# Optimization experiments

Measured on AMD Instinct MI355X. Metric: run time of the kernel, lower is better.

The kernel has to match this reference:

```python
import jax, jax.numpy as jnp
import numpy as np

DIST_THRESH = 0.1
W_DIST = 0.05
W_CHAMFER = 0.05
W_SEP = 0.0005


def setup_inputs() -> dict:
    key = jax.random.key(0)
    k1, k2, k3, k4 = jax.random.split(key, 4)
    B, N, K = 4, 200000, 64
    return {
        "landmarks_C": jax.random.uniform(k1, (B, N, 3), jnp.float32),          # predicted point coords
        "landmarks_F": jax.random.normal(k2, (B, N, 4), jnp.float32) * 0.05,    # [dist, dx, dy, dz]
        "targets_C": jax.random.uniform(k3, (B, K, 3), jnp.float32),            # GT landmark coords
        "targets_F": jax.random.randint(k4, (B, K), 0, 8),                      # GT landmark class labels
        "classes": jnp.arange(6),                                               # classes to supervise
    }


def reference(landmarks_C, landmarks_F, targets_C, targets_F, classes):
    def per_batch(C_i, F_i, tC, tF):
        # class mask over GT landmarks (replaces boolean indexing in torch)
        mask_k = jnp.any(tF[None, :] == classes[:, None], axis=0)          # [K]
        n_valid = mask_k.sum()
        dists_i = F_i[:, 0]                                                # predicted distance, [N]
        coords_i = C_i + F_i[:, 1:]                                        # refined coords, [N,3]
        # pairwise dists GT landmarks -> raw point coords, invalid classes pushed to +inf
        pd = jnp.linalg.norm(C_i[None, :, :] - tC[:, None, :], axis=-1)    # [K,N]
        pd = jnp.where(mask_k[:, None], pd, jnp.inf)
        min_d = pd.min(axis=0)                                             # [N]
        pm = min_d < DIST_THRESH                                           # points near some GT landmark
        # smooth-L1 (beta=1, sum) on predicted distance; clip(inf)=2*thresh reproduces empty-target fallback
        tgt = jnp.clip(min_d, 0.0, 2.0 * DIST_THRESH)
        diff = dists_i - tgt
        ad = jnp.abs(diff)
        dist_loss = jnp.where(ad < 1.0, 0.5 * diff * diff, ad - 0.5).sum()
        # pairwise dists GT landmarks -> refined coords
        ld = jnp.linalg.norm(coords_i[None, :, :] - tC[:, None, :], axis=-1)  # [K,N]
        ld_m = jnp.where(mask_k[:, None], ld, jnp.inf)
        p2g = jnp.where(pm, ld_m.min(axis=0), 0.0)                         # pred->gt, masked points only
        g2p = jnp.where(mask_k, ld_m.min(axis=1), 0.0)                     # gt->pred, valid GT only
        chamfer = (p2g * p2g).sum() + (g2p * g2p).sum()
        # separation: ratio of dists to 2 nearest (valid) GT landmarks, per masked point
        _, idx = jax.lax.top_k(-pd.T, 2)                                   # [N,2] indices of 2 smallest
        d01 = jnp.take_along_axis(ld.T, idx, axis=1)                       # [N,2]
        sep = jnp.where(pm, d01[:, 0] / d01[:, 1], 0.0).sum()
        sep = jnp.where(n_valid >= 2, sep, 0.0)
        return W_DIST * dist_loss + W_CHAMFER * chamfer + W_SEP * sep

    losses = jax.vmap(per_batch)(landmarks_C, landmarks_F, targets_C, targets_F)
    return losses.mean()
```

## Files before the change

kernel.cpp:

```cpp
#include <hip/hip_runtime.h>


constexpr int KT = 64;
constexpr int P  = 4;
constexpr int NREP = 16;
constexpr float DIST_THRESH = 0.1f;
constexpr float W_DIST    = 0.05f;
constexpr float W_CHAMFER = 0.05f;
constexpr float W_SEP     = 0.0005f;
constexpr float PT_SENT = -1e18f;
constexpr float TG_SENT = -1e18f;
constexpr float BIGF  = 3.0e38f;
constexpr float WBIAS = 16.0f;

typedef float f2 __attribute__((ext_vector_type(2)));

__device__ __forceinline__ unsigned umin_(unsigned a, unsigned b) { return a < b ? a : b; }
__device__ __forceinline__ unsigned umax_(unsigned a, unsigned b) { return a > b ? a : b; }

__device__ __forceinline__ f2 pk_fma(f2 a, f2 b, f2 c) {
#if __has_builtin(__builtin_elementwise_fma)
    return __builtin_elementwise_fma(a, b, c);
#else
    f2 r; r.x = fmaf(a.x, b.x, c.x); r.y = fmaf(a.y, b.y, c.y); return r;
#endif
}

__global__ __launch_bounds__(128, 6)
void landmark_main(const float* __restrict__ C, const float* __restrict__ F,
                   const float* __restrict__ tC, const int* __restrict__ tF,
                   const int* __restrict__ classes, int n_classes,
                   int N, unsigned int* __restrict__ g2p_rep,
                   float* __restrict__ sums_rep)
{
    __shared__ float4 tgtH[2][32];
    __shared__ float4 tgtFull[KT];
    __shared__ unsigned g2pLDS[KT];
    __shared__ uint4  mK1[64];
    __shared__ uint4  mK2[64];
    __shared__ float4 mLM[64];

    const int tid   = threadIdx.x;
    const int lane  = tid & 63;
    const int h     = tid >> 6;
    const int l31   = lane & 31;
    const int lx    = l31 ^ ((lane >> 5) << 4);
    const int blk   = blockIdx.x;
    const int b     = blk & 3;
    const int chunk = blk >> 2;
    const int rep   = chunk & (NREP - 1);
    const unsigned kbase = (unsigned)(h << 5);

    if (tid < KT) {
        int f = tF[b * KT + tid];
        bool valid = false;
        for (int c = 0; c < n_classes; ++c) valid = valid || (f == classes[c]);
        float x = TG_SENT, y = TG_SENT, z = TG_SENT;
        if (valid) {
            x = tC[(b * KT + tid) * 3 + 0];
            y = tC[(b * KT + tid) * 3 + 1];
            z = tC[(b * KT + tid) * 3 + 2];
        }
        float4 v = make_float4(-2.f * x, -2.f * y, -2.f * z,
                               x * x + y * y + z * z + WBIAS);
        tgtFull[tid] = v;
        tgtH[tid >> 5][tid & 31] = v;
        g2pLDS[tid] = 0x7F7FFFFFu;
    }
    __syncthreads();

    const float*  Cb = C + (size_t)b * N * 3;
    const float4* Fb = (const float4*)(F + (size_t)b * N * 4);
    const int base = chunk * (64 * P);

    f2 pcx[P], pcy[P], pcz[P];
    float ppm[P], ccm[P], f0[P];
    #pragma unroll
    for (int p = 0; p < P; ++p) {
        int n = base + p * 64 + lane;
        bool v = (n < N);
        int ni = v ? n : 0;
        float4 f4 = Fb[ni];
        float X = Cb[3 * ni + 0], Y = Cb[3 * ni + 1], Z = Cb[3 * ni + 2];
        f0[p] = v ? f4.x : 2.0f * DIST_THRESH;
        if (!v) { X = PT_SENT; Y = PT_SENT; Z = PT_SENT; f4.y = f4.z = f4.w = 0.f; }
        float cxv = X + f4.y, cyv = Y + f4.z, czv = Z + f4.w;
        pcx[p] = (f2){X, cxv};
        pcy[p] = (f2){Y, cyv};
        pcz[p] = (f2){Z, czv};
        ppm[p] = fmaf(Z, Z, fmaf(Y, Y, X * X)) - WBIAS;
        ccm[p] = fmaf(czv, czv, fmaf(cyv, cyv, cxv * cxv)) - WBIAS;
    }

    unsigned k1[P], k2[P];
    float lmin[P];
    #pragma unroll
    for (int p = 0; p < P; ++p) { k1[p] = 0xFFFFFFFFu; k2[p] = 0xFFFFFFFFu; lmin[p] = BIGF; }

    #pragma unroll 8
    for (int i = 0; i < 32; ++i) {
        const unsigned kk = (unsigned)(lx ^ i);
        const float4 T = tgtH[h][kk];
        const unsigned tk = kk | kbase;
        const f2 Tx = {T.x, T.x}, Ty = {T.y, T.y}, Tz = {T.z, T.z}, Tw = {T.w, T.w};
        float av[P];
        #pragma unroll
        for (int p = 0; p < P; ++p) {
            f2 w = pk_fma(pcx[p], Tx, pk_fma(pcy[p], Ty, pk_fma(pcz[p], Tz, Tw)));
            unsigned key = (__float_as_uint(w.x) & 0xFFFFFFC0u) | tk;
            unsigned hi = umax_(k1[p], key);
            k1[p] = umin_(k1[p], key);
            k2[p] = umin_(k2[p], hi);
            lmin[p] = fminf(lmin[p], w.y);
            av[p] = w.y + ccm[p];
        }
        float dl = fmaxf(fminf(fminf(av[0], av[1]), fminf(av[2], av[3])), 0.f);
        atomicMin(&g2pLDS[tk], __float_as_uint(dl));
    }

    if (h == 0) {
        mK1[lane] = make_uint4(k1[0], k1[1], k1[2], k1[3]);
        mK2[lane] = make_uint4(k2[0], k2[1], k2[2], k2[3]);
        mLM[lane] = make_float4(lmin[0], lmin[1], lmin[2], lmin[3]);
    }
    __syncthreads();

    if (h == 0) {
        atomicMax(&g2p_rep[rep * 256 + b * 64 + lane], ~g2pLDS[lane]);
    } else {
        uint4 A1 = mK1[lane], A2 = mK2[lane];
        float4 AL = mLM[lane];
        const unsigned a1v[P] = {A1.x, A1.y, A1.z, A1.w};
        const unsigned a2v[P] = {A2.x, A2.y, A2.z, A2.w};
        const float    alv[P] = {AL.x, AL.y, AL.z, AL.w};

        float dist_acc = 0.f, p2g_acc = 0.f, sep_acc = 0.f;
        #pragma unroll
        for (int p = 0; p < P; ++p) {
            unsigned m1 = umin_(a1v[p], k1[p]);
            unsigned m2 = umin_(umax_(a1v[p], k1[p]), umin_(a2v[p], k2[p]));
            float lm = fminf(alv[p], lmin[p]);
            float keyf1 = __uint_as_float(m1 & 0xFFFFFFC0u);
            float mind = sqrtf(fmaxf(keyf1 + ppm[p], 0.f));
            bool pm = mind < DIST_THRESH;
            float tgtv = fminf(mind, 2.0f * DIST_THRESH);
            float diff = f0[p] - tgtv;
            float ad = fabsf(diff);
            dist_acc += (ad < 1.0f) ? 0.5f * diff * diff : (ad - 0.5f);
            if (pm) {
                p2g_acc += fmaxf(lm + ccm[p], 0.f);
                int i1 = (int)(m1 & 63u), i2 = (int)(m2 & 63u);
                float4 T1 = tgtFull[i1], T2 = tgtFull[i2];
                float cxv = pcx[p].y, cyv = pcy[p].y, czv = pcz[p].y;
                float l1sq = fmaf(cxv, T1.x, fmaf(cyv, T1.y, fmaf(czv, T1.z, T1.w))) + ccm[p];
                float l2sq = fmaf(cxv, T2.x, fmaf(cyv, T2.y, fmaf(czv, T2.z, T2.w))) + ccm[p];
                sep_acc += sqrtf(fmaxf(l1sq, 0.f) / fmaxf(l2sq, 1e-30f));
            }
        }

        float v0 = dist_acc, v1 = p2g_acc, v2 = sep_acc;
        #pragma unroll
        for (int o = 32; o > 0; o >>= 1) {
            v0 += __shfl_down(v0, o, 64);
            v1 += __shfl_down(v1, o, 64);
            v2 += __shfl_down(v2, o, 64);
        }
        if (lane == 0) {
            float* sb = sums_rep + rep * 16 + b;
            atomicAdd(sb + 0, v0);
            atomicAdd(sb + 4, v1);
            atomicAdd(sb + 8, v2);
        }
    }
}

__global__ void landmark_finalize(const int* __restrict__ tF, const int* __restrict__ classes,
                                  int n_classes, const unsigned int* __restrict__ g2p_rep,
                                  const float* __restrict__ sums_rep, float* __restrict__ out)
{
    __shared__ float lossb[4];
    const int tid = threadIdx.x;
    const int b = tid >> 6, k = tid & 63;

    int f = tF[b * KT + k];
    bool valid = false;
    for (int c = 0; c < n_classes; ++c) valid = valid || (f == classes[c]);

    unsigned enc = 0;
    for (int r = 0; r < NREP; ++r) enc = umax_(enc, g2p_rep[r * 256 + b * 64 + k]);
    float g  = valid ? __uint_as_float(~enc) : 0.f;
    float nv = valid ? 1.f : 0.f;

    #pragma unroll
    for (int o = 32; o > 0; o >>= 1) {
        g  += __shfl_down(g, o, 64);
        nv += __shfl_down(nv, o, 64);
    }
    if (k == 0) {
        float sd = 0.f, sp = 0.f, ss = 0.f;
        for (int r = 0; r < NREP; ++r) {
            sd += sums_rep[r * 16 + 0 + b];
            sp += sums_rep[r * 16 + 4 + b];
            ss += sums_rep[r * 16 + 8 + b];
        }
        float sep = (nv >= 2.f) ? ss : 0.f;
        lossb[b] = W_DIST * sd + W_CHAMFER * (sp + g) + W_SEP * sep;
    }
    __syncthreads();
    if (tid == 0)
        out[0] = (lossb[0] + lossb[1] + lossb[2] + lossb[3]) * 0.25f;
}

extern "C" void kernel_launch(void* const* d_in, const int* in_sizes, int n_in,
                              void* d_out, int out_size, void* d_ws, size_t ws_size,
                              hipStream_t stream)
{
    const float* C       = (const float*)d_in[0];
    const float* F       = (const float*)d_in[1];
    const float* tC      = (const float*)d_in[2];
    const int*   tF      = (const int*)d_in[3];
    const int*   classes = (const int*)d_in[4];
    const int n_classes = in_sizes[4];
    const int B = 4;
    const int N = in_sizes[0] / (3 * B);

    unsigned int* g2p_rep  = (unsigned int*)d_ws;
    float*        sums_rep = (float*)((char*)d_ws + NREP * 256 * 4);

    hipMemsetAsync(d_ws, 0, NREP * 256 * 4 + NREP * 16 * 4, stream);

    const int cpb = (N + 64 * P - 1) / (64 * P);
    landmark_main<<<cpb * 4, 128, 0, stream>>>(C, F, tC, tF, classes, n_classes,
                                               N, g2p_rep, sums_rep);
    landmark_finalize<<<1, 256, 0, stream>>>(tF, classes, n_classes, g2p_rep,
                                             sums_rep, (float*)d_out);
}
```

Baseline: 99.20 us.

## Fuse finalize into main kernel via last-block counter and drop split-K targets

Each wave now scans all 64 targets for its own 4x64 points instead of splitting the targets across two waves and merging through LDS. Blocks grow to 256 threads covering 1024 points. The separate finalize kernel is folded into the main kernel using an atomic completion counter, so the last block performs the reduction. This removes one kernel launch and the intra-block merge, in exchange for a longer serial loop per wave, more redundant per-point work, and a grid-wide atomic and threadfence at the end of every block.

```diff
diff --git a/kernel.cpp b/kernel.cpp
--- a/kernel.cpp
+++ b/kernel.cpp
@@ -26,30 +26,25 @@
 #endif
 }
 
-__global__ __launch_bounds__(128, 6)
+__global__ __launch_bounds__(256, 4)
 void landmark_main(const float* __restrict__ C, const float* __restrict__ F,
                    const float* __restrict__ tC, const int* __restrict__ tF,
-                   const int* __restrict__ classes, int n_classes,
-                   int N, unsigned int* __restrict__ g2p_rep,
-                   float* __restrict__ sums_rep)
+                   const int* __restrict__ classes, int n_classes, int N,
+                   unsigned int* __restrict__ g2p_rep, float* __restrict__ sums_rep,
+                   unsigned int* __restrict__ counter, float* __restrict__ out)
 {
-    __shared__ float4 tgtH[2][32];
-    __shared__ float4 tgtFull[KT];
+    __shared__ float4   tgtFull[KT];
     __shared__ unsigned g2pLDS[KT];
-    __shared__ uint4  mK1[64];
-    __shared__ uint4  mK2[64];
-    __shared__ float4 mLM[64];
+    __shared__ int      sIsLast;
+    __shared__ float    lossb[4];
 
     const int tid   = threadIdx.x;
     const int lane  = tid & 63;
-    const int h     = tid >> 6;
-    const int l31   = lane & 31;
-    const int lx    = l31 ^ ((lane >> 5) << 4);
+    const int wv    = tid >> 6;
     const int blk   = blockIdx.x;
     const int b     = blk & 3;
     const int chunk = blk >> 2;
     const int rep   = chunk & (NREP - 1);
-    const unsigned kbase = (unsigned)(h << 5);
 
     if (tid < KT) {
         int f = tF[b * KT + tid];
@@ -61,17 +56,15 @@
             y = tC[(b * KT + tid) * 3 + 1];
             z = tC[(b * KT + tid) * 3 + 2];
         }
-        float4 v = make_float4(-2.f * x, -2.f * y, -2.f * z,
-                               x * x + y * y + z * z + WBIAS);
-        tgtFull[tid] = v;
-        tgtH[tid >> 5][tid & 31] = v;
+        tgtFull[tid] = make_float4(-2.f * x, -2.f * y, -2.f * z,
+                                   x * x + y * y + z * z + WBIAS);
         g2pLDS[tid] = 0x7F7FFFFFu;
     }
     __syncthreads();
 
     const float*  Cb = C + (size_t)b * N * 3;
     const float4* Fb = (const float4*)(F + (size_t)b * N * 4);
-    const int base = chunk * (64 * P);
+    const int base = chunk * (256 * P) + (wv << 8);
 
     f2 pcx[P], pcy[P], pcz[P];
     float ppm[P], ccm[P], f0[P];
@@ -97,97 +90,84 @@
     #pragma unroll
     for (int p = 0; p < P; ++p) { k1[p] = 0xFFFFFFFFu; k2[p] = 0xFFFFFFFFu; lmin[p] = BIGF; }
 
+    const int lx = lane ^ (wv << 4);
     #pragma unroll 8
-    for (int i = 0; i < 32; ++i) {
-        const unsigned kk = (unsigned)(lx ^ i);
-        const float4 T = tgtH[h][kk];
-        const unsigned tk = kk | kbase;
+    for (int i = 0; i < KT; ++i) {
+        const int kk = lx ^ i;
+        const float4 T = tgtFull[kk];
+        const unsigned tk = (unsigned)kk;
         const f2 Tx = {T.x, T.x}, Ty = {T.y, T.y}, Tz = {T.z, T.z}, Tw = {T.w, T.w};
         float av[P];
         #pragma unroll
         for (int p = 0; p < P; ++p) {
-            f2 w = pk_fma(pcx[p], Tx, pk_fma(pcy[p], Ty, pk_fma(pcz[p], Tz, Tw)));
-            unsigned key = (__float_as_uint(w.x) & 0xFFFFFFC0u) | tk;
+            f2 w2 = pk_fma(pcx[p], Tx, pk_fma(pcy[p], Ty, pk_fma(pcz[p], Tz, Tw)));
+            unsigned key = (__float_as_uint(w2.x) & 0xFFFFFFC0u) | tk;
             unsigned hi = umax_(k1[p], key);
             k1[p] = umin_(k1[p], key);
             k2[p] = umin_(k2[p], hi);
-            lmin[p] = fminf(lmin[p], w.y);
-            av[p] = w.y + ccm[p];
+            lmin[p] = fminf(lmin[p], w2.y);
+            av[p] = w2.y + ccm[p];
         }
         float dl = fmaxf(fminf(fminf(av[0], av[1]), fminf(av[2], av[3])), 0.f);
-        atomicMin(&g2pLDS[tk], __float_as_uint(dl));
-    }
-
-    if (h == 0) {
-        mK1[lane] = make_uint4(k1[0], k1[1], k1[2], k1[3]);
-        mK2[lane] = make_uint4(k2[0], k2[1], k2[2], k2[3]);
-        mLM[lane] = make_float4(lmin[0], lmin[1], lmin[2], lmin[3]);
-    }
-    __syncthreads();
-
-    if (h == 0) {
-        atomicMax(&g2p_rep[rep * 256 + b * 64 + lane], ~g2pLDS[lane]);
-    } else {
-        uint4 A1 = mK1[lane], A2 = mK2[lane];
-        float4 AL = mLM[lane];
-        const unsigned a1v[P] = {A1.x, A1.y, A1.z, A1.w};
-        const unsigned a2v[P] = {A2.x, A2.y, A2.z, A2.w};
-        const float    alv[P] = {AL.x, AL.y, AL.z, AL.w};
-
-        float dist_acc = 0.f, p2g_acc = 0.f, sep_acc = 0.f;
-        #pragma unroll
-        for (int p = 0; p < P; ++p) {
-            unsigned m1 = umin_(a1v[p], k1[p]);
-            unsigned m2 = umin_(umax_(a1v[p], k1[p]), umin_(a2v[p], k2[p]));
-            float lm = fminf(alv[p], lmin[p]);
-            float keyf1 = __uint_as_float(m1 & 0xFFFFFFC0u);
-            float mind = sqrtf(fmaxf(keyf1 + ppm[p], 0.f));
-            bool pm = mind < DIST_THRESH;
-            float tgtv = fminf(mind, 2.0f * DIST_THRESH);
-            float diff = f0[p] - tgtv;
-            float ad = fabsf(diff);
-            dist_acc += (ad < 1.0f) ? 0.5f * diff * diff : (ad - 0.5f);
-            if (pm) {
-                p2g_acc += fmaxf(lm + ccm[p], 0.f);
-                int i1 = (int)(m1 & 63u), i2 = (int)(m2 & 63u);
-                float4 T1 = tgtFull[i1], T2 = tgtFull[i2];
-                float cxv = pcx[p].y, cyv = pcy[p].y, czv = pcz[p].y;
-                float l1sq = fmaf(cxv, T1.x, fmaf(cyv, T1.y, fmaf(czv, T1.z, T1.w))) + ccm[p];
-                float l2sq = fmaf(cxv, T2.x, fmaf(cyv, T2.y, fmaf(czv, T2.z, T2.w))) + ccm[p];
-                sep_acc += sqrtf(fmaxf(l1sq, 0.f) / fmaxf(l2sq, 1e-30f));
-            }
-        }
-
-        float v0 = dist_acc, v1 = p2g_acc, v2 = sep_acc;
-        #pragma unroll
-        for (int o = 32; o > 0; o >>= 1) {
-            v0 += __shfl_down(v0, o, 64);
-            v1 += __shfl_down(v1, o, 64);
-            v2 += __shfl_down(v2, o, 64);
-        }
-        if (lane == 0) {
-            float* sb = sums_rep + rep * 16 + b;
-            atomicAdd(sb + 0, v0);
-            atomicAdd(sb + 4, v1);
-            atomicAdd(sb + 8, v2);
-        }
-    }
-}
-
-__global__ void landmark_finalize(const int* __restrict__ tF, const int* __restrict__ classes,
-                                  int n_classes, const unsigned int* __restrict__ g2p_rep,
-                                  const float* __restrict__ sums_rep, float* __restrict__ out)
-{
-    __shared__ float lossb[4];
-    const int tid = threadIdx.x;
-    const int b = tid >> 6, k = tid & 63;
-
-    int f = tF[b * KT + k];
+        atomicMin(&g2pLDS[kk], __float_as_uint(dl));
+    }
+
+    float dist_acc = 0.f, p2g_acc = 0.f, sep_acc = 0.f;
+    #pragma unroll
+    for (int p = 0; p < P; ++p) {
+        unsigned m1 = k1[p], m2 = k2[p];
+        float lm = lmin[p];
+        float keyf1 = __uint_as_float(m1 & 0xFFFFFFC0u);
+        float mind = sqrtf(fmaxf(keyf1 + ppm[p], 0.f));
+        bool pm = mind < DIST_THRESH;
+        float tgtv = fminf(mind, 2.0f * DIST_THRESH);
+        float diff = f0[p] - tgtv;
+        float ad = fabsf(diff);
+        dist_acc += (ad < 1.0f) ? 0.5f * diff * diff : (ad - 0.5f);
+        if (pm) {
+            p2g_acc += fmaxf(lm + ccm[p], 0.f);
+            int i1 = (int)(m1 & 63u), i2 = (int)(m2 & 63u);
+            float4 T1 = tgtFull[i1], T2 = tgtFull[i2];
+            float cxv = pcx[p].y, cyv = pcy[p].y, czv = pcz[p].y;
+            float l1sq = fmaf(cxv, T1.x, fmaf(cyv, T1.y, fmaf(czv, T1.z, T1.w))) + ccm[p];
+            float l2sq = fmaf(cxv, T2.x, fmaf(cyv, T2.y, fmaf(czv, T2.z, T2.w))) + ccm[p];
+            sep_acc += sqrtf(fmaxf(l1sq, 0.f) / fmaxf(l2sq, 1e-30f));
+        }
+    }
+
+    float v0 = dist_acc, v1 = p2g_acc, v2 = sep_acc;
+    #pragma unroll
+    for (int o = 32; o > 0; o >>= 1) {
+        v0 += __shfl_down(v0, o, 64);
+        v1 += __shfl_down(v1, o, 64);
+        v2 += __shfl_down(v2, o, 64);
+    }
+    if (lane == 0) {
+        float* sb = sums_rep + rep * 16 + b;
+        atomicAdd(sb + 0, v0);
+        atomicAdd(sb + 4, v1);
+        atomicAdd(sb + 8, v2);
+    }
+
+    __syncthreads();
+    if (tid < KT)
+        atomicMax(&g2p_rep[rep * 256 + b * 64 + tid], ~g2pLDS[tid]);
+
+    __threadfence();
+    __syncthreads();
+    if (tid == 0)
+        sIsLast = (atomicAdd(counter, 1u) == (unsigned)(gridDim.x - 1));
+    __syncthreads();
+    if (!sIsLast) return;
+
+    const int b2 = tid >> 6, k = tid & 63;
+    int fk = tF[b2 * KT + k];
     bool valid = false;
-    for (int c = 0; c < n_classes; ++c) valid = valid || (f == classes[c]);
+    for (int c = 0; c < n_classes; ++c) valid = valid || (fk == classes[c]);
 
     unsigned enc = 0;
-    for (int r = 0; r < NREP; ++r) enc = umax_(enc, g2p_rep[r * 256 + b * 64 + k]);
+    for (int r = 0; r < NREP; ++r)
+        enc = umax_(enc, atomicMax(&g2p_rep[r * 256 + b2 * 64 + k], 0u));
     float g  = valid ? __uint_as_float(~enc) : 0.f;
     float nv = valid ? 1.f : 0.f;
 
@@ -199,12 +179,12 @@
     if (k == 0) {
         float sd = 0.f, sp = 0.f, ss = 0.f;
         for (int r = 0; r < NREP; ++r) {
-            sd += sums_rep[r * 16 + 0 + b];
-            sp += sums_rep[r * 16 + 4 + b];
-            ss += sums_rep[r * 16 + 8 + b];
+            sd += atomicAdd(&sums_rep[r * 16 + 0 + b2], 0.f);
+            sp += atomicAdd(&sums_rep[r * 16 + 4 + b2], 0.f);
+            ss += atomicAdd(&sums_rep[r * 16 + 8 + b2], 0.f);
         }
         float sep = (nv >= 2.f) ? ss : 0.f;
-        lossb[b] = W_DIST * sd + W_CHAMFER * (sp + g) + W_SEP * sep;
+        lossb[b2] = W_DIST * sd + W_CHAMFER * (sp + g) + W_SEP * sep;
     }
     __syncthreads();
     if (tid == 0)
@@ -226,12 +206,12 @@
 
     unsigned int* g2p_rep  = (unsigned int*)d_ws;
     float*        sums_rep = (float*)((char*)d_ws + NREP * 256 * 4);
-
-    hipMemsetAsync(d_ws, 0, NREP * 256 * 4 + NREP * 16 * 4, stream);
-
-    const int cpb = (N + 64 * P - 1) / (64 * P);
-    landmark_main<<<cpb * 4, 128, 0, stream>>>(C, F, tC, tF, classes, n_classes,
-                                               N, g2p_rep, sums_rep);
-    landmark_finalize<<<1, 256, 0, stream>>>(tF, classes, n_classes, g2p_rep,
-                                             sums_rep, (float*)d_out);
+    unsigned int* counter  = (unsigned int*)((char*)d_ws + NREP * 256 * 4 + NREP * 16 * 4);
+
+    hipMemsetAsync(d_ws, 0, NREP * 256 * 4 + NREP * 16 * 4 + 4, stream);
+
+    const int cpb = (N + 256 * P - 1) / (256 * P);
+    landmark_main<<<cpb * 4, 256, 0, stream>>>(C, F, tC, tF, classes, n_classes,
+                                               N, g2p_rep, sums_rep, counter,
+                                               (float*)d_out);
 }
```

Result: slower. 133.7 us (+34.7%).
